# Kernel tuning notes

Measured on AMD Instinct MI355X. Metric: run time of the kernel, lower is better.

Reference implementation:

```python
import jax, jax.numpy as jnp
import numpy as np

DIM = 1024
NUM_HEADS = 16
HEAD_DIM = DIM // NUM_HEADS  # 64; only used for the softmax scale


def setup_inputs() -> dict:
    key = jax.random.key(0)
    ks = jax.random.split(key, 9)
    s = 1.0 / np.sqrt(DIM)
    return {
        "x": jax.random.normal(ks[0], (2, 4096, DIM), dtype=jnp.float32),
        "Wq": jax.random.normal(ks[1], (DIM, DIM), dtype=jnp.float32) * s,
        "bq": jnp.zeros((DIM,), dtype=jnp.float32),
        "Wk": jax.random.normal(ks[2], (DIM, DIM), dtype=jnp.float32) * s,
        "bk": jnp.zeros((DIM,), dtype=jnp.float32),
        "Wv": jax.random.normal(ks[3], (DIM, DIM), dtype=jnp.float32) * s,
        "bv": jnp.zeros((DIM,), dtype=jnp.float32),
        "Wo": jax.random.normal(ks[4], (DIM, DIM), dtype=jnp.float32) * s,
        "bo": jnp.zeros((DIM,), dtype=jnp.float32),
    }


def reference(x, Wq, bq, Wk, bk, Wv, bv, Wo, bo):
    # Projections (nn.Linear equivalents)
    q = jnp.einsum("bsd,df->bsf", x, Wq) + bq
    k = jnp.einsum("bsd,df->bsf", x, Wk) + bk
    v = jnp.einsum("bsd,df->bsf", x, Wv) + bv
    # Full-dim attention (no head split); scale uses head_dim per original code.
    scale = 1.0 / np.sqrt(HEAD_DIM)
    scores = jnp.einsum("bqd,bkd->bqk", q, k) * scale  # [B, S, S]
    attn = jax.nn.softmax(scores, axis=-1)
    out = jnp.einsum("bqk,bkd->bqd", attn, v)
    return jnp.einsum("bsd,df->bsf", out, Wo) + bo
```

## Files before the change

### kernel.cpp

```cpp
#include <hip/hip_runtime.h>

typedef unsigned short u16;
using bf16x8  = __attribute__((ext_vector_type(8))) __bf16;
using floatx4 = __attribute__((ext_vector_type(4))) float;

__device__ __forceinline__ u16 f2bf(float f) {
  unsigned int u = __builtin_bit_cast(unsigned int, f);
  u += 0x7fffu + ((u >> 16) & 1u);
  return (u16)(u >> 16);
}
__device__ __forceinline__ float bf2f(u16 h) {
  unsigned int u = ((unsigned int)h) << 16;
  return __builtin_bit_cast(float, u);
}

#define AS1(p) ((const __attribute__((address_space(1))) void*)(p))
#define AS3(p) ((__attribute__((address_space(3))) void*)(p))

#define GEMM_PROLOGUE_AT(bmv, bnv)                                           \
  __shared__ u16 As[128 * 32];                                               \
  __shared__ u16 Bs[128 * 32];                                               \
  const int tid  = threadIdx.x;                                              \
  const int wave = tid >> 6, lane = tid & 63;                                \
  const int wm = (wave >> 1) * 64, wn = (wave & 1) * 64;                     \
  const long bm = (bmv), bn = (bnv);                                         \
  floatx4 acc[4][4] = {};                                                    \
  const int srow = lane >> 2;                                                \
  const int scol = (lane & 3) * 8;                                           \
  const int c0 = wave * 2, c1 = c0 + 1;                                      \
  const int fr = lane & 15;                                                  \
  const int kq = (lane >> 4) * 8;                                            \
  const int oc = (lane >> 4) * 4;

#define GEMM_PROLOGUE() GEMM_PROLOGUE_AT((long)blockIdx.y * 128, (long)blockIdx.x * 128)

#define GEMM_STAGE(Ab, Bb, K, k0)                                            \
    __syncthreads();                                                         \
    __builtin_amdgcn_global_load_lds(AS1(Ab + (long)(c0*16 + srow)*K + k0 + scol), AS3(As + c0*512), 16, 0, 0); \
    __builtin_amdgcn_global_load_lds(AS1(Ab + (long)(c1*16 + srow)*K + k0 + scol), AS3(As + c1*512), 16, 0, 0); \
    __builtin_amdgcn_global_load_lds(AS1(Bb + (long)(c0*16 + srow)*K + k0 + scol), AS3(Bs + c0*512), 16, 0, 0); \
    __builtin_amdgcn_global_load_lds(AS1(Bb + (long)(c1*16 + srow)*K + k0 + scol), AS3(Bs + c1*512), 16, 0, 0); \
    __syncthreads();                                                         \
    bf16x8 af[4], bfv[4];                                                    \
    _Pragma("unroll")                                                        \
    for (int mi = 0; mi < 4; ++mi)                                           \
      af[mi] = *(const bf16x8*)(As + (wm + mi*16 + fr)*32 + kq);             \
    _Pragma("unroll")                                                        \
    for (int ni = 0; ni < 4; ++ni)                                           \
      bfv[ni] = *(const bf16x8*)(Bs + (wn + ni*16 + fr)*32 + kq);

#define GEMM_KSTEP(Ab, Bb, K, k0)                                            \
  {                                                                          \
    GEMM_STAGE(Ab, Bb, K, k0)                                                \
    _Pragma("unroll")                                                        \
    for (int mi = 0; mi < 4; ++mi)                                           \
      _Pragma("unroll")                                                      \
      for (int ni = 0; ni < 4; ++ni)                                         \
        acc[mi][ni] = __builtin_amdgcn_mfma_f32_16x16x32_bf16(af[mi], bfv[ni], acc[mi][ni], 0, 0, 0); \
  }

#define GEMM_KSTEP_SWAP(Ab, Bb, K, k0)                                       \
  {                                                                          \
    GEMM_STAGE(Ab, Bb, K, k0)                                                \
    _Pragma("unroll")                                                        \
    for (int mi = 0; mi < 4; ++mi)                                           \
      _Pragma("unroll")                                                      \
      for (int ni = 0; ni < 4; ++ni)                                         \
        acc[mi][ni] = __builtin_amdgcn_mfma_f32_16x16x32_bf16(bfv[ni], af[mi], acc[mi][ni], 0, 0, 0); \
  }

#define NE_PROLOGUE(bmv, bnv)                                                \
  __shared__ u16 lds[65536];                                    \
  const int tid = threadIdx.x;                                               \
  const int w = tid >> 6, lane = tid & 63;                                   \
  const int wm = (w >> 2) * 128, wn = (w & 3) * 64;                          \
  const int wm16 = (w >> 2) * 8;           \
  const int wn4  = (w & 3) * 4;            \
  const long bm = (bmv), bn = (bnv);                                         \
  floatx4 acc[8][4] = {};                                                    \
  const int fr = lane & 15;                                                  \
  const int kq = (lane >> 4) * 8;                                            \
  const int oc = (lane >> 4) * 4;                                            \
         \
  const int swz  = (lane * 16) ^ (((lane >> 5) & 1) << 5);                   \
  const int srow = swz >> 6;                  \
  const int scol = (swz & 63) >> 1;           \
  const int st0  = w * 2;                      \
                        \
  const int aoff = fr * 64 + ((kq * 2) ^ (((fr >> 3) & 1) << 5));

#define NE_SETUP_PTRS(Abp, Bbp, ldK)                                         \
  const u16* A0p = (Abp) + (long)(st0 * 16 + srow) * (ldK) + scol;           \
  const u16* A1p = A0p + 16L * (ldK);                                        \
  const u16* B0p = (Bbp) + (long)(st0 * 16 + srow) * (ldK) + scol;           \
  const u16* B1p = B0p + 16L * (ldK);

#define NE_SA(T)                                                             \
  { u16* d_ = lds + (((T) & 3) * 16384) + st0 * 512;                         \
    long o_ = (long)(T) * 32;                                                \
    __builtin_amdgcn_global_load_lds(AS1(A0p + o_), AS3(d_), 16, 0, 0);      \
    __builtin_amdgcn_global_load_lds(AS1(A1p + o_), AS3(d_ + 512), 16, 0, 0); }
#define NE_SB(T)                                                             \
  { u16* d_ = lds + (((T) & 3) * 16384) + 8192 + st0 * 512;                  \
    long o_ = (long)(T) * 32;                                                \
    __builtin_amdgcn_global_load_lds(AS1(B0p + o_), AS3(d_), 16, 0, 0);      \
    __builtin_amdgcn_global_load_lds(AS1(B1p + o_), AS3(d_ + 512), 16, 0, 0); }

#define NE_TILE(T, NT)                                                       \
  {                                                                          \
    const char* sb_ = (const char*)lds + ((T) & 3) * 32768;                  \
    bf16x8 af[4], bf[4];                                                     \
    _Pragma("unroll")                                                        \
    for (int i = 0; i < 4; ++i)                                              \
      af[i] = *(const bf16x8*)(sb_ + (wm16 + i) * 1024 + aoff);              \
    _Pragma("unroll")                                                        \
    for (int i = 0; i < 4; ++i)                                              \
      bf[i] = *(const bf16x8*)(sb_ + 16384 + (wn4 + i) * 1024 + aoff);       \
    if ((T) + 2 < (NT)) NE_SB((T) + 2)                                       \
    __builtin_amdgcn_s_barrier();                                            \
    asm volatile("s_waitcnt lgkmcnt(0)" ::: "memory");                       \
    __builtin_amdgcn_sched_barrier(0);                                       \
    __builtin_amdgcn_s_setprio(1);                                           \
    _Pragma("unroll")                                                        \
    for (int mi = 0; mi < 4; ++mi)                                           \
      _Pragma("unroll")                                                      \
      for (int ni = 0; ni < 4; ++ni)                                         \
        acc[mi][ni] = __builtin_amdgcn_mfma_f32_16x16x32_bf16(bf[ni], af[mi], acc[mi][ni], 0, 0, 0); \
    __builtin_amdgcn_s_setprio(0);                                           \
    __builtin_amdgcn_s_barrier();                                            \
    __builtin_amdgcn_sched_barrier(0);                                       \
    _Pragma("unroll")                                                        \
    for (int i = 0; i < 4; ++i)                                              \
      af[i] = *(const bf16x8*)(sb_ + (wm16 + 4 + i) * 1024 + aoff);          \
    if ((T) + 3 < (NT)) NE_SA((T) + 3)                                       \
    __builtin_amdgcn_s_barrier();                                            \
    asm volatile("s_waitcnt lgkmcnt(0)" ::: "memory");                       \
    __builtin_amdgcn_sched_barrier(0);                                       \
    __builtin_amdgcn_s_setprio(1);                                           \
    _Pragma("unroll")                                                        \
    for (int mi = 0; mi < 4; ++mi)                                           \
      _Pragma("unroll")                                                      \
      for (int ni = 0; ni < 4; ++ni)                                         \
        acc[4 + mi][ni] = __builtin_amdgcn_mfma_f32_16x16x32_bf16(bf[ni], af[mi], acc[4 + mi][ni], 0, 0, 0); \
    __builtin_amdgcn_s_setprio(0);                                           \
    if ((T) < (NT) - 3)       { asm volatile("s_waitcnt vmcnt(6)" ::: "memory"); } \
    else if ((T) == (NT) - 3) { asm volatile("s_waitcnt vmcnt(4)" ::: "memory"); } \
    else if ((T) == (NT) - 2) { asm volatile("s_waitcnt vmcnt(0)" ::: "memory"); } \
    __builtin_amdgcn_s_barrier();                                            \
    __builtin_amdgcn_sched_barrier(0);                                       \
  }

#define NE_START()                                                           \
  NE_SA(0) NE_SB(0) NE_SA(1) NE_SB(1) NE_SA(2)                               \
  asm volatile("s_waitcnt vmcnt(6)" ::: "memory");                           \
  __builtin_amdgcn_s_barrier();                                              \
  __builtin_amdgcn_sched_barrier(0);

__global__ __launch_bounds__(256) void gemm_bt(
    const u16* __restrict__ A, const u16* __restrict__ Bt,
    float* __restrict__ Cout, const float* __restrict__ bias, int N, int K)
{
  GEMM_PROLOGUE();
  const u16* Ab = A + bm * K;
  const u16* Bb = Bt + bn * K;
  for (int k0 = 0; k0 < K; k0 += 32) GEMM_KSTEP_SWAP(Ab, Bb, K, k0);

#pragma unroll
  for (int mi = 0; mi < 4; ++mi) {
    long row = bm + wm + mi*16 + fr;
#pragma unroll
    for (int ni = 0; ni < 4; ++ni) {
      long colb = bn + wn + ni*16 + oc;
      float4 bv4 = *(const float4*)(bias + colb);
      float4 o;
      o.x = acc[mi][ni][0] + bv4.x;
      o.y = acc[mi][ni][1] + bv4.y;
      o.z = acc[mi][ni][2] + bv4.z;
      o.w = acc[mi][ni][3] + bv4.w;
      *(float4*)(Cout + row * N + colb) = o;
    }
  }
}

__global__ __launch_bounds__(512, 2) void gemm_qk_exp(
    const u16* __restrict__ q, const u16* __restrict__ k,
    u16* __restrict__ probs, float* __restrict__ lpartT, float alpha)
{
  const int N = 4096;
  const int xcd = blockIdx.x;
  const int j = blockIdx.y;
  const long b = xcd >> 2;
  const int by = (xcd & 3) * 4 + (j & 3);
  const int bx = j >> 2;

  NE_PROLOGUE((long)by * 256, (long)bx * 256);
  const u16* Ab = q + b * 4096 * 1024 + bm * 1024;
  const u16* Bb = k + b * 4096 * 1024 + bn * 1024;
  NE_SETUP_PTRS(Ab, Bb, 1024);
  u16* P = probs + b * 4096L * 4096;
  float* lp = lpartT + b * 4096 * 64;

  NE_START()
  for (int T = 0; T < 32; ++T) NE_TILE(T, 32)

  const float a2 = alpha * 1.44269504f;
  const int cg = bx * 4 + (w & 3);
#pragma unroll
  for (int mi = 0; mi < 8; ++mi) {
    long row = bm + wm + mi * 16 + fr;
    float rs = 0.f;
#pragma unroll
    for (int ni = 0; ni < 4; ++ni) {
      long colb = bn + wn + ni * 16 + oc;
      float e0 = __builtin_amdgcn_exp2f(acc[mi][ni][0] * a2);
      float e1 = __builtin_amdgcn_exp2f(acc[mi][ni][1] * a2);
      float e2 = __builtin_amdgcn_exp2f(acc[mi][ni][2] * a2);
      float e3 = __builtin_amdgcn_exp2f(acc[mi][ni][3] * a2);
      rs += (e0 + e1) + (e2 + e3);
      ushort4 o;
      o.x = f2bf(e0); o.y = f2bf(e1); o.z = f2bf(e2); o.w = f2bf(e3);
      *(ushort4*)(P + row * N + colb) = o;
    }
    rs += __shfl_xor(rs, 16);
    rs += __shfl_xor(rs, 32);
    if (lane < 16)
      lp[(bm + wm + mi * 16 + lane) * 64 + cg] = rs;
  }
}

__global__ __launch_bounds__(512, 2) void gemm_pv_splitk2(
    const u16* __restrict__ probs, const u16* __restrict__ vT,
    u16* __restrict__ pA, u16* __restrict__ pB)
{
  const int xcd = blockIdx.x;
  const int j = blockIdx.y;
  const long b = xcd >> 2;
  const int sp = (xcd >> 1) & 1;
  const int by = (xcd & 1) * 8 + (j & 7);
  const int bx = j >> 3;

  NE_PROLOGUE((long)by * 256, (long)bx * 256);
  const u16* Ab = probs + b * 4096L * 4096 + bm * 4096 + sp * 2048;
  const u16* Bb = vT + b * 1024L * 4096 + bn * 4096 + sp * 2048;
  NE_SETUP_PTRS(Ab, Bb, 4096);
  u16* part = (b ? pB : pA) + (long)sp * 4096 * 1024;

  NE_START()
  for (int T = 0; T < 64; ++T) NE_TILE(T, 64)

#pragma unroll
  for (int mi = 0; mi < 8; ++mi) {
    long row = bm + wm + mi * 16 + fr;
#pragma unroll
    for (int ni = 0; ni < 4; ++ni) {
      long colb = bn + wn + ni * 16 + oc;
      ushort4 o;
      o.x = f2bf(acc[mi][ni][0]);
      o.y = f2bf(acc[mi][ni][1]);
      o.z = f2bf(acc[mi][ni][2]);
      o.w = f2bf(acc[mi][ni][3]);
      *(ushort4*)(part + row * 1024 + colb) = o;
    }
  }
}

__global__ __launch_bounds__(256) void gemm_qkv(
    const u16* __restrict__ A, const u16* __restrict__ Bt,
    u16* __restrict__ qb, u16* __restrict__ kb, u16* __restrict__ vT,
    const float* __restrict__ bq, const float* __restrict__ bk,
    const float* __restrict__ bv)
{
  const int K = 1024;
  GEMM_PROLOGUE();
  const u16* Ab = A + bm * K;
  const u16* Bb = Bt + bn * K;

  if (bn < 2048) {
    for (int k0 = 0; k0 < K; k0 += 32) GEMM_KSTEP_SWAP(Ab, Bb, K, k0);
    u16* C = (bn < 1024) ? qb : kb;
    const float* bias = (bn < 1024) ? bq : bk;
#pragma unroll
    for (int mi = 0; mi < 4; ++mi) {
      long row = bm + wm + mi*16 + fr;
#pragma unroll
      for (int ni = 0; ni < 4; ++ni) {
        long colg = bn + wn + ni*16 + oc;
        long cc = colg & 1023;
        float4 bv4 = *(const float4*)(bias + cc);
        ushort4 o;
        o.x = f2bf(acc[mi][ni][0] + bv4.x);
        o.y = f2bf(acc[mi][ni][1] + bv4.y);
        o.z = f2bf(acc[mi][ni][2] + bv4.z);
        o.w = f2bf(acc[mi][ni][3] + bv4.w);
        *(ushort4*)(C + row * 1024 + cc) = o;
      }
    }
  } else {
    for (int k0 = 0; k0 < K; k0 += 32) GEMM_KSTEP(Ab, Bb, K, k0);
    const int orow = (lane >> 4) * 4;
    const int ocol = lane & 15;
#pragma unroll
    for (int ni = 0; ni < 4; ++ni) {
      long col = bn + wn + ni*16 + ocol;
      float bvv = bv[col - 2048];
#pragma unroll
      for (int mi = 0; mi < 4; ++mi) {
        long row = bm + wm + mi*16 + orow;
        long b_ = row >> 12, s = row & 4095, d = col - 2048;
        ushort4 o;
        o.x = f2bf(acc[mi][ni][0] + bvv);
        o.y = f2bf(acc[mi][ni][1] + bvv);
        o.z = f2bf(acc[mi][ni][2] + bvv);
        o.w = f2bf(acc[mi][ni][3] + bvv);
        *(ushort4*)(vT + b_ * (1024L * 4096) + d * 4096L + s) = o;
      }
    }
  }
}

__global__ __launch_bounds__(256) void reduce2_div_row(
    const u16* __restrict__ pA, const u16* __restrict__ pB,
    const float* __restrict__ lpartT, u16* __restrict__ ob)
{
  const int row = blockIdx.x;
  const long b = blockIdx.y;
  const int tid = threadIdx.x;
  const u16* part = b ? pB : pA;
  const float* lp = lpartT + b * 4096 * 64;
  __shared__ float sl;
  if (tid < 64) {
    float s = lp[(long)row * 64 + tid];
#pragma unroll
    for (int off = 32; off; off >>= 1) s += __shfl_down(s, off);
    if (tid == 0) sl = s;
  }
  __syncthreads();
  const float inv = 1.0f / sl;
  const long base = (long)row * 1024 + tid * 4;
  float acc4[4] = {0.f, 0.f, 0.f, 0.f};
#pragma unroll
  for (int s = 0; s < 2; ++s) {
    ushort4 p = *(const ushort4*)(part + (long)s * 4096 * 1024 + base);
    acc4[0] += bf2f(p.x); acc4[1] += bf2f(p.y);
    acc4[2] += bf2f(p.z); acc4[3] += bf2f(p.w);
  }
  ushort4 o;
  o.x = f2bf(acc4[0] * inv);
  o.y = f2bf(acc4[1] * inv);
  o.z = f2bf(acc4[2] * inv);
  o.w = f2bf(acc4[3] * inv);
  *(ushort4*)(ob + b * 4096L * 1024 + base) = o;
}

__global__ __launch_bounds__(256) void prep(
    const float* __restrict__ x, u16* __restrict__ xb,
    const float* __restrict__ W0, const float* __restrict__ W1,
    const float* __restrict__ W2, const float* __restrict__ W3,
    u16* __restrict__ O0, u16* __restrict__ O1,
    u16* __restrict__ O2, u16* __restrict__ O3)
{
  __shared__ float tile[32][33];
  int blk = blockIdx.x;
  if (blk < 8192) {
    int i = blk * 256 + threadIdx.x;
    float4 f = ((const float4*)x)[i];
    ushort4 o;
    o.x = f2bf(f.x); o.y = f2bf(f.y); o.z = f2bf(f.z); o.w = f2bf(f.w);
    ((ushort4*)xb)[i] = o;
  } else {
    blk -= 8192;
    const int z = blk >> 10, t = blk & 1023;
    const float* in = (z == 0) ? W0 : (z == 1) ? W1 : (z == 2) ? W2 : W3;
    u16* outp = (z == 0) ? O0 : (z == 1) ? O1 : (z == 2) ? O2 : O3;
    const int bx = (t & 31) * 32, by = (t >> 5) * 32;
    const int tx = threadIdx.x & 31, ty = threadIdx.x >> 5;
    for (int i = ty; i < 32; i += 8)
      tile[i][tx] = in[(long)(by + i) * 1024 + bx + tx];
    __syncthreads();
    for (int i = ty; i < 32; i += 8)
      outp[(long)(bx + i) * 1024 + by + tx] = f2bf(tile[tx][i]);
  }
}

extern "C" void kernel_launch(void* const* d_in, const int* in_sizes, int n_in,
                              void* d_out, int out_size, void* d_ws, size_t ws_size,
                              hipStream_t stream) {
  const float* x  = (const float*)d_in[0];
  const float* Wq = (const float*)d_in[1];
  const float* bq = (const float*)d_in[2];
  const float* Wk = (const float*)d_in[3];
  const float* bk = (const float*)d_in[4];
  const float* Wv = (const float*)d_in[5];
  const float* bv = (const float*)d_in[6];
  const float* Wo = (const float*)d_in[7];
  const float* bo = (const float*)d_in[8];
  float* out = (float*)d_out;

  const int B = 2, S = 4096, D = 1024;
  const long MS = (long)B * S;
  const long MB = 1L << 20;

  char* w = (char*)d_ws;
  u16* qb  = (u16*)(w);
  u16* kb  = (u16*)(w + 16 * MB);
  u16* vT  = (u16*)(w + 32 * MB);
  u16* xb  = (u16*)(w + 48 * MB);
  u16* ob  = xb;
  u16* WqkvT = (u16*)(w + 64 * MB);
  u16* WoT = WqkvT + 3072L * 1024;
  u16* probs = (u16*)(w + 72 * MB);
  u16* partA = (u16*)(w);
  u16* partB = (u16*)(w + 136 * MB);
  float* lpartT = (float*)d_out;

  prep<<<dim3(8192 + 4096), 256, 0, stream>>>(
      x, xb, Wq, Wk, Wv, Wo,
      WqkvT, WqkvT + 1024L * 1024, WqkvT + 2048L * 1024, WoT);

  gemm_qkv<<<dim3(3 * D / 128, MS / 128), 256, 0, stream>>>(
      xb, WqkvT, qb, kb, vT, bq, bk, bv);

  const float scale = 0.125f;
  gemm_qk_exp<<<dim3(8, 64), 512, 0, stream>>>(
      qb, kb, probs, lpartT, scale);
  gemm_pv_splitk2<<<dim3(8, 32), 512, 0, stream>>>(
      probs, vT, partA, partB);
  reduce2_div_row<<<dim3(S, B), 256, 0, stream>>>(partA, partB, lpartT, ob);

  gemm_bt<<<dim3(D / 128, MS / 128), 256, 0, stream>>>(ob, WoT, out, bo, D, D);
}
```

Measured before the change: 385.2 us.

## Port QKV projection GEMM to 256x256 pipelined tile kernel with XCD-aware block mapping

Replaces the simple 128x128, 256-thread, single-buffered GEMM for the fused QKV projection with the 256x256, 512-thread, 4-stage global_load_lds pipelined tile scheme already used by the attention GEMMs. A non-swapped MFMA variant handles the V block so it can be stored transposed. Block indices are remapped so consecutive row tiles land on the same XCD, aiming at better L2 reuse. The larger tiles cut redundant global traffic and sync stalls but reduce grid size to 384 blocks and raise register and LDS pressure.

New measurement: 375.1 us. 2.6% less time.

```diff
diff --git a/kernel.cpp b/kernel.cpp
--- a/kernel.cpp
+++ b/kernel.cpp
@@ -48,16 +48,6 @@
     _Pragma("unroll")                                                        \
     for (int ni = 0; ni < 4; ++ni)                                           \
       bfv[ni] = *(const bf16x8*)(Bs + (wn + ni*16 + fr)*32 + kq);
-
-#define GEMM_KSTEP(Ab, Bb, K, k0)                                            \
-  {                                                                          \
-    GEMM_STAGE(Ab, Bb, K, k0)                                                \
-    _Pragma("unroll")                                                        \
-    for (int mi = 0; mi < 4; ++mi)                                           \
-      _Pragma("unroll")                                                      \
-      for (int ni = 0; ni < 4; ++ni)                                         \
-        acc[mi][ni] = __builtin_amdgcn_mfma_f32_16x16x32_bf16(af[mi], bfv[ni], acc[mi][ni], 0, 0, 0); \
-  }
 
 #define GEMM_KSTEP_SWAP(Ab, Bb, K, k0)                                       \
   {                                                                          \
@@ -106,7 +96,7 @@
     __builtin_amdgcn_global_load_lds(AS1(B0p + o_), AS3(d_), 16, 0, 0);      \
     __builtin_amdgcn_global_load_lds(AS1(B1p + o_), AS3(d_ + 512), 16, 0, 0); }
 
-#define NE_TILE(T, NT)                                                       \
+#define NE_TILE_G(T, NT, MF)                                                 \
   {                                                                          \
     const char* sb_ = (const char*)lds + ((T) & 3) * 32768;                  \
     bf16x8 af[4], bf[4];                                                     \
@@ -125,7 +115,7 @@
     for (int mi = 0; mi < 4; ++mi)                                           \
       _Pragma("unroll")                                                      \
       for (int ni = 0; ni < 4; ++ni)                                         \
-        acc[mi][ni] = __builtin_amdgcn_mfma_f32_16x16x32_bf16(bf[ni], af[mi], acc[mi][ni], 0, 0, 0); \
+        acc[mi][ni] = MF(mi, ni, acc[mi][ni]);                               \
     __builtin_amdgcn_s_setprio(0);                                           \
     __builtin_amdgcn_s_barrier();                                            \
     __builtin_amdgcn_sched_barrier(0);                                       \
@@ -141,7 +131,7 @@
     for (int mi = 0; mi < 4; ++mi)                                           \
       _Pragma("unroll")                                                      \
       for (int ni = 0; ni < 4; ++ni)                                         \
-        acc[4 + mi][ni] = __builtin_amdgcn_mfma_f32_16x16x32_bf16(bf[ni], af[mi], acc[4 + mi][ni], 0, 0, 0); \
+        acc[4 + mi][ni] = MF(mi, ni, acc[4 + mi][ni]);                       \
     __builtin_amdgcn_s_setprio(0);                                           \
     if ((T) < (NT) - 3)       { asm volatile("s_waitcnt vmcnt(6)" ::: "memory"); } \
     else if ((T) == (NT) - 3) { asm volatile("s_waitcnt vmcnt(4)" ::: "memory"); } \
@@ -149,6 +139,11 @@
     __builtin_amdgcn_s_barrier();                                            \
     __builtin_amdgcn_sched_barrier(0);                                       \
   }
+
+#define NE_MF_SWAP(mi, ni, c) __builtin_amdgcn_mfma_f32_16x16x32_bf16(bf[ni], af[mi], (c), 0, 0, 0)
+#define NE_MF_NS(mi, ni, c)   __builtin_amdgcn_mfma_f32_16x16x32_bf16(af[mi], bf[ni], (c), 0, 0, 0)
+#define NE_TILE(T, NT)    NE_TILE_G(T, NT, NE_MF_SWAP)
+#define NE_TILE_NS(T, NT) NE_TILE_G(T, NT, NE_MF_NS)
 
 #define NE_START()                                                           \
   NE_SA(0) NE_SB(0) NE_SA(1) NE_SB(1) NE_SA(2)                               \
@@ -264,27 +259,33 @@
   }
 }
 
-__global__ __launch_bounds__(256) void gemm_qkv(
+__global__ __launch_bounds__(512, 2) void gemm_qkv(
     const u16* __restrict__ A, const u16* __restrict__ Bt,
     u16* __restrict__ qb, u16* __restrict__ kb, u16* __restrict__ vT,
     const float* __restrict__ bq, const float* __restrict__ bk,
     const float* __restrict__ bv)
 {
-  const int K = 1024;
-  GEMM_PROLOGUE();
-  const u16* Ab = A + bm * K;
-  const u16* Bb = Bt + bn * K;
+  const int xcd = blockIdx.x;
+  const int j = blockIdx.y;
+  const int by = xcd * 4 + (j & 3);
+  const int bx = j >> 2;
+
+  NE_PROLOGUE((long)by * 256, (long)bx * 256);
+  const u16* Ab = A + bm * 1024;
+  const u16* Bb = Bt + bn * 1024;
+  NE_SETUP_PTRS(Ab, Bb, 1024);
 
   if (bn < 2048) {
-    for (int k0 = 0; k0 < K; k0 += 32) GEMM_KSTEP_SWAP(Ab, Bb, K, k0);
+    NE_START()
+    for (int T = 0; T < 32; ++T) NE_TILE(T, 32)
     u16* C = (bn < 1024) ? qb : kb;
     const float* bias = (bn < 1024) ? bq : bk;
 #pragma unroll
-    for (int mi = 0; mi < 4; ++mi) {
-      long row = bm + wm + mi*16 + fr;
+    for (int mi = 0; mi < 8; ++mi) {
+      long row = bm + wm + mi * 16 + fr;
 #pragma unroll
       for (int ni = 0; ni < 4; ++ni) {
-        long colg = bn + wn + ni*16 + oc;
+        long colg = bn + wn + ni * 16 + oc;
         long cc = colg & 1023;
         float4 bv4 = *(const float4*)(bias + cc);
         ushort4 o;
@@ -296,23 +297,25 @@
       }
     }
   } else {
-    for (int k0 = 0; k0 < K; k0 += 32) GEMM_KSTEP(Ab, Bb, K, k0);
+    NE_START()
+    for (int T = 0; T < 32; ++T) NE_TILE_NS(T, 32)
     const int orow = (lane >> 4) * 4;
-    const int ocol = lane & 15;
+    const long b_ = bm >> 12;
+    const long s0 = (bm & 4095) + wm;
+    u16* vb = vT + b_ * (1024L * 4096);
 #pragma unroll
     for (int ni = 0; ni < 4; ++ni) {
-      long col = bn + wn + ni*16 + ocol;
-      float bvv = bv[col - 2048];
-#pragma unroll
-      for (int mi = 0; mi < 4; ++mi) {
-        long row = bm + wm + mi*16 + orow;
-        long b_ = row >> 12, s = row & 4095, d = col - 2048;
+      long d = bn + wn + ni * 16 + fr - 2048;
+      float bvv = bv[d];
+#pragma unroll
+      for (int mi = 0; mi < 8; ++mi) {
+        long s = s0 + mi * 16 + orow;
         ushort4 o;
         o.x = f2bf(acc[mi][ni][0] + bvv);
         o.y = f2bf(acc[mi][ni][1] + bvv);
         o.z = f2bf(acc[mi][ni][2] + bvv);
         o.w = f2bf(acc[mi][ni][3] + bvv);
-        *(ushort4*)(vT + b_ * (1024L * 4096) + d * 4096L + s) = o;
+        *(ushort4*)(vb + d * 4096L + s) = o;
       }
     }
   }
@@ -417,7 +420,7 @@
       x, xb, Wq, Wk, Wv, Wo,
       WqkvT, WqkvT + 1024L * 1024, WqkvT + 2048L * 1024, WoT);
 
-  gemm_qkv<<<dim3(3 * D / 128, MS / 128), 256, 0, stream>>>(
+  gemm_qkv<<<dim3(8, 48), 512, 0, stream>>>(
       xb, WqkvT, qb, kb, vT, bq, bk, bv);
 
   const float scale = 0.125f;
```
